# Performance work log

Hardware: AMD Instinct MI355X
Metric: run time of the kernel (lower is better)

Reference implementation:

```python
import jax, jax.numpy as jnp
import numpy as np

B, S, E, H = 2, 2048, 1024, 16
D = E // H  # head_dim = 64


def setup_inputs() -> dict:
    key = jax.random.key(0)
    ks = jax.random.split(key, 6)
    sc = 1.0 / np.sqrt(D)
    return {
        "x": jax.random.normal(ks[0], (B, S, E), dtype=jnp.float32),
        "Wq": jax.random.normal(ks[1], (D, D), dtype=jnp.float32) * sc,
        "Wk": jax.random.normal(ks[2], (D, D), dtype=jnp.float32) * sc,
        "Wv": jax.random.normal(ks[3], (D, D), dtype=jnp.float32) * sc,
        "Wo": jax.random.normal(ks[4], (E, E), dtype=jnp.float32) * (1.0 / np.sqrt(E)),
        "bo": jnp.zeros((E,), dtype=jnp.float32),
    }


def reference(x, Wq, Wk, Wv, Wo, bo):
    b, s, e = x.shape
    # split into heads: (B, H, S, D)
    xh = x.reshape(b, s, H, D).transpose(0, 2, 1, 3)
    # per-head linear projections (weights SHARED across heads); torch Linear: x @ W^T
    q = jnp.einsum('bhsd,ed->bhse', xh, Wq)
    k = jnp.einsum('bhsd,ed->bhse', xh, Wk)
    v = jnp.einsum('bhsd,ed->bhse', xh, Wv)
    # full attention matrix (B, H, S, S) — faithful to the naive original
    energy = jnp.einsum('bhqd,bhkd->bhqk', q, k)
    attn = jax.nn.softmax(energy / jnp.sqrt(jnp.asarray(D, x.dtype)), axis=-1)
    out = jnp.einsum('bhqk,bhkd->bhqd', attn, v)
    out = out.transpose(0, 2, 1, 3).reshape(b, s, e)
    return out @ Wo.T + bo
```

## Files before the change

kernel.cpp:

```cpp
#include <hip/hip_runtime.h>
#include <hip/hip_bf16.h>

#define B 2
#define S 2048
#define E 1024
#define H 16
#define D 64

typedef unsigned short ushort_t;
typedef __attribute__((ext_vector_type(8))) short bf16x8;
typedef __attribute__((ext_vector_type(4))) float f32x4;
typedef __attribute__((ext_vector_type(16))) float f32x16;

static __device__ __forceinline__ ushort_t f2bf(float f) {
    union { float f; unsigned u; } v; v.f = f;
    unsigned r = v.u + 0x7fffu + ((v.u >> 16) & 1u);
    return (ushort_t)(r >> 16);
}

#define MFMA(a, b, c)   __builtin_amdgcn_mfma_f32_16x16x32_bf16((a), (b), (c), 0, 0, 0)
#define MFMA32(a, b, c) __builtin_amdgcn_mfma_f32_32x32x16_bf16((a), (b), (c), 0, 0, 0)
#define PACKBF(hi, lo) __builtin_amdgcn_perm((hi), (lo), 0x07060302u)

__global__ __launch_bounds__(256) void cvt_w(
    const float* __restrict__ Wq, const float* __restrict__ Wk, const float* __restrict__ Wv,
    const float* __restrict__ Wo,
    ushort_t* __restrict__ wqb, ushort_t* __restrict__ wkb, ushort_t* __restrict__ wvb,
    ushort_t* __restrict__ wob)
{
    int gid = blockIdx.x, t = threadIdx.x;
    if (gid < 1024) {
        int i = gid * 1024 + t * 4;
        float4 f = *(const float4*)(Wo + i);
        ushort4 u; u.x = f2bf(f.x); u.y = f2bf(f.y); u.z = f2bf(f.z); u.w = f2bf(f.w);
        *(ushort4*)(wob + i) = u;
    } else {
        int idx = (gid - 1024) * 1024 + t * 4;
        int which = idx >> 12, off = idx & 4095;
        const float* src = (which == 0) ? Wq : (which == 1) ? Wk : Wv;
        ushort_t* dst    = (which == 0) ? wqb : (which == 1) ? wkb : wvb;
        float sc = (which == 0) ? 0.18033688011112042f : 1.0f;
        float4 f = *(const float4*)(src + off);
        ushort4 u; u.x = f2bf(f.x * sc); u.y = f2bf(f.y * sc);
        u.z = f2bf(f.z * sc); u.w = f2bf(f.w * sc);
        *(ushort4*)(dst + off) = u;
    }
}

__global__ __launch_bounds__(256) void qkv_proj(
    const float* __restrict__ x,
    const ushort_t* __restrict__ wq, const ushort_t* __restrict__ wk, const ushort_t* __restrict__ wv,
    ushort_t* __restrict__ q, ushort_t* __restrict__ k, ushort_t* __restrict__ vT)
{
    __shared__ ushort_t Xs[64][72];
    __shared__ ushort_t Wqs[64][72], Wks[64][72], Wvs[64][72];
    int t = threadIdx.x;
    int bh = blockIdx.y, b = bh >> 4, h = bh & 15;
    int s0 = blockIdx.x * 64;

    {
        int i = t >> 2, d0 = (t & 3) * 16;
        const float* xp = x + ((size_t)(b * S + s0 + i)) * E + h * D + d0;
        #pragma unroll
        for (int c = 0; c < 16; c += 4) {
            float4 f = *(const float4*)(xp + c);
            Xs[i][d0 + c + 0] = f2bf(f.x); Xs[i][d0 + c + 1] = f2bf(f.y);
            Xs[i][d0 + c + 2] = f2bf(f.z); Xs[i][d0 + c + 3] = f2bf(f.w);
        }
    }
    {
        int e = t >> 2, d0 = (t & 3) * 16;
        *(bf16x8*)&Wqs[e][d0]     = *(const bf16x8*)(wq + e * 64 + d0);
        *(bf16x8*)&Wqs[e][d0 + 8] = *(const bf16x8*)(wq + e * 64 + d0 + 8);
        *(bf16x8*)&Wks[e][d0]     = *(const bf16x8*)(wk + e * 64 + d0);
        *(bf16x8*)&Wks[e][d0 + 8] = *(const bf16x8*)(wk + e * 64 + d0 + 8);
        *(bf16x8*)&Wvs[e][d0]     = *(const bf16x8*)(wv + e * 64 + d0);
        *(bf16x8*)&Wvs[e][d0 + 8] = *(const bf16x8*)(wv + e * 64 + d0 + 8);
    }
    __syncthreads();

    int w = t >> 6, lane = t & 63, m = lane & 15, quad = lane >> 4;
    bf16x8 a0 = *(bf16x8*)&Xs[16 * w + m][quad * 8];
    bf16x8 a1 = *(bf16x8*)&Xs[16 * w + m][32 + quad * 8];
    f32x4 cq[4], ck[4], cv[4];
    #pragma unroll
    for (int nt = 0; nt < 4; nt++) { cq[nt] = (f32x4)0.f; ck[nt] = (f32x4)0.f; cv[nt] = (f32x4)0.f; }
    #pragma unroll
    for (int nt = 0; nt < 4; nt++) {
        bf16x8 b0, b1;
        b0 = *(bf16x8*)&Wqs[nt * 16 + m][quad * 8]; b1 = *(bf16x8*)&Wqs[nt * 16 + m][32 + quad * 8];
        cq[nt] = MFMA(a0, b0, cq[nt]); cq[nt] = MFMA(a1, b1, cq[nt]);
        b0 = *(bf16x8*)&Wks[nt * 16 + m][quad * 8]; b1 = *(bf16x8*)&Wks[nt * 16 + m][32 + quad * 8];
        ck[nt] = MFMA(a0, b0, ck[nt]); ck[nt] = MFMA(a1, b1, ck[nt]);
        b0 = *(bf16x8*)&Wvs[nt * 16 + m][quad * 8]; b1 = *(bf16x8*)&Wvs[nt * 16 + m][32 + quad * 8];
        cv[nt] = MFMA(a0, b0, cv[nt]); cv[nt] = MFMA(a1, b1, cv[nt]);
    }
    size_t base = (size_t)bh * S + s0;
    #pragma unroll
    for (int nt = 0; nt < 4; nt++)
        #pragma unroll
        for (int r = 0; r < 4; r++) {
            size_t idx = (base + 16 * w + quad * 4 + r) * D + nt * 16 + m;
            q[idx] = f2bf(cq[nt][r]);
            k[idx] = f2bf(ck[nt][r]);
        }
    __syncthreads();
    #pragma unroll
    for (int nt = 0; nt < 4; nt++)
        #pragma unroll
        for (int r = 0; r < 4; r++)
            Wvs[nt * 16 + m][16 * w + quad * 4 + r] = f2bf(cv[nt][r]);
    __syncthreads();
    {
        int d0 = t >> 2, sc = (t & 3) * 16;
        ushort_t* vp = vT + ((size_t)bh * D + d0) * S + s0 + sc;
        *(bf16x8*)(vp)     = *(bf16x8*)&Wvs[d0][sc];
        *(bf16x8*)(vp + 8) = *(bf16x8*)&Wvs[d0][sc + 8];
    }
}

__global__ __launch_bounds__(256) void flash_attn(
    const ushort_t* __restrict__ q, const ushort_t* __restrict__ k,
    const ushort_t* __restrict__ vT, ushort_t* __restrict__ ao)
{
    __shared__ ushort_t Ks[2][64][72];
    __shared__ ushort_t Vt[2][64][72];
    int t = threadIdx.x;
    int bh = blockIdx.y, b = bh >> 4, h = bh & 15;
    int q0 = blockIdx.x * 128;
    int w = t >> 6, lane = t & 63, l31 = lane & 31, half = lane >> 5;

    const ushort_t* qb = q + ((size_t)bh * S + q0) * D;
    const ushort_t* kb = k + (size_t)bh * S * D;
    const ushort_t* vb = vT + (size_t)bh * D * S;

    bf16x8 qf[4];
    {
        const ushort_t* qp = qb + (size_t)(w * 32 + l31) * D + half * 8;
        #pragma unroll
        for (int c = 0; c < 4; c++) qf[c] = *(const bf16x8*)(qp + c * 16);
    }

    f32x16 o0 = (f32x16)0.f, o1 = (f32x16)0.f;
    float2 ls2 = make_float2(0.f, 0.f);

    int sr = t >> 2, scc = (t & 3) * 16;
    bf16x8 kp0, kp1, vp0, vp1;

    {
        const ushort_t* kp = kb + (size_t)sr * D + scc;
        const ushort_t* vp = vb + (size_t)sr * S + scc;
        kp0 = *(const bf16x8*)(kp);     kp1 = *(const bf16x8*)(kp + 8);
        vp0 = *(const bf16x8*)(vp);     vp1 = *(const bf16x8*)(vp + 8);
        *(bf16x8*)&Ks[0][sr][scc]     = kp0;
        *(bf16x8*)&Ks[0][sr][scc + 8] = kp1;
        *(bf16x8*)&Vt[0][sr][scc]     = vp0;
        *(bf16x8*)&Vt[0][sr][scc + 8] = vp1;
    }
    __syncthreads();
    {
        const ushort_t* kp = kb + (size_t)(64 + sr) * D + scc;
        const ushort_t* vp = vb + (size_t)sr * S + 64 + scc;
        kp0 = *(const bf16x8*)(kp);     kp1 = *(const bf16x8*)(kp + 8);
        vp0 = *(const bf16x8*)(vp);     vp1 = *(const bf16x8*)(vp + 8);
    }

    const int NT = S / 64;
    for (int it = 0; it < NT; it++) {
        int p = it & 1;
        if (it + 1 < NT) {
            *(bf16x8*)&Ks[1 - p][sr][scc]     = kp0;
            *(bf16x8*)&Ks[1 - p][sr][scc + 8] = kp1;
            *(bf16x8*)&Vt[1 - p][sr][scc]     = vp0;
            *(bf16x8*)&Vt[1 - p][sr][scc + 8] = vp1;
        }
        if (it + 2 < NT) {
            int k0n = (it + 2) * 64;
            const ushort_t* kp = kb + (size_t)(k0n + sr) * D + scc;
            const ushort_t* vp = vb + (size_t)sr * S + k0n + scc;
            kp0 = *(const bf16x8*)(kp);     kp1 = *(const bf16x8*)(kp + 8);
            vp0 = *(const bf16x8*)(vp);     vp1 = *(const bf16x8*)(vp + 8);
        }

        union { unsigned u[4]; bf16x8 v; } pa[4];
        #pragma unroll
        for (int st = 0; st < 2; st++) {
            f32x16 e = (f32x16)0.f;
            #pragma unroll
            for (int c = 0; c < 4; c++) {
                bf16x8 ka = *(bf16x8*)&Ks[p][st * 32 + l31][c * 16 + half * 8];
                e = MFMA32(ka, qf[c], e);
            }
            unsigned pt[16];
            #pragma unroll
            for (int r = 0; r < 16; r += 2) {
                float pe0 = __builtin_amdgcn_exp2f(e[r]);
                float pe1 = __builtin_amdgcn_exp2f(e[r + 1]);
                ls2.x += pe0; ls2.y += pe1;
                pt[r]     = __float_as_uint(pe0);
                pt[r + 1] = __float_as_uint(pe1);
            }
            #pragma unroll
            for (int c2 = 0; c2 < 2; c2++) {
                int rb = c2 * 8;
                unsigned dA = PACKBF(pt[rb + 1], pt[rb + 0]);
                unsigned dB = PACKBF(pt[rb + 3], pt[rb + 2]);
                unsigned dC = PACKBF(pt[rb + 5], pt[rb + 4]);
                unsigned dD = PACKBF(pt[rb + 7], pt[rb + 6]);
                unsigned x1 = (unsigned)__shfl_xor((int)(half ? dA : dC), 32, 64);
                unsigned x2 = (unsigned)__shfl_xor((int)(half ? dB : dD), 32, 64);
                int kc = st * 2 + c2;
                pa[kc].u[0] = half ? x1 : dA;
                pa[kc].u[1] = half ? x2 : dB;
                pa[kc].u[2] = half ? dC : x1;
                pa[kc].u[3] = half ? dD : x2;
            }
        }

        #pragma unroll
        for (int kc = 0; kc < 4; kc++) {
            bf16x8 vf0 = *(bf16x8*)&Vt[p][l31][kc * 16 + half * 8];
            bf16x8 vf1 = *(bf16x8*)&Vt[p][32 + l31][kc * 16 + half * 8];
            o0 = MFMA32(pa[kc].v, vf0, o0);
            o1 = MFMA32(pa[kc].v, vf1, o1);
        }
        __syncthreads();
    }

    float lsum = ls2.x + ls2.y;
    float lfull = lsum + __shfl_xor(lsum, 32, 64);
    float inv = 1.001953125f / lfull;
    #pragma unroll
    for (int reg = 0; reg < 16; reg++) {
        int qrow = (reg & 3) + 8 * (reg >> 2) + 4 * half;
        float li = __shfl(inv, qrow, 64);
        int srow = q0 + w * 32 + qrow;
        size_t base = ((size_t)(b * S + srow)) * E + h * D + l31;
        ao[base]      = f2bf(o0[reg] * li);
        ao[base + 32] = f2bf(o1[reg] * li);
    }
}

__global__ __launch_bounds__(256) void out_proj(
    const ushort_t* __restrict__ A, const ushort_t* __restrict__ Wob,
    const float* __restrict__ bo, float* __restrict__ Y)
{
    __shared__ ushort_t As[2][128][72];
    __shared__ ushort_t Ws[2][64][72];
    int t = threadIdx.x;
    int n0 = blockIdx.x * 64, m0 = blockIdx.y * 128;
    int w = t >> 6, lane = t & 63, m = lane & 15, quad = lane >> 4;
    f32x4 acc[2][4];
    #pragma unroll
    for (int u = 0; u < 2; u++)
        #pragma unroll
        for (int nt = 0; nt < 4; nt++) acc[u][nt] = (f32x4)0.f;

    int ar = t >> 1, ac = (t & 1) * 32;
    int wr = t >> 2, wc = (t & 3) * 16;
    const ushort_t* apb = A + (size_t)(m0 + ar) * E + ac;
    const ushort_t* wpb = Wob + (size_t)(n0 + wr) * E + wc;

    bf16x8 arg[4], wrg[2];
    {
        #pragma unroll
        for (int i = 0; i < 4; i++) *(bf16x8*)&As[0][ar][ac + 8 * i] = *(const bf16x8*)(apb + 8 * i);
        *(bf16x8*)&Ws[0][wr][wc]     = *(const bf16x8*)(wpb);
        *(bf16x8*)&Ws[0][wr][wc + 8] = *(const bf16x8*)(wpb + 8);
    }
    __syncthreads();
    {
        #pragma unroll
        for (int i = 0; i < 4; i++) arg[i] = *(const bf16x8*)(apb + 64 + 8 * i);
        wrg[0] = *(const bf16x8*)(wpb + 64);
        wrg[1] = *(const bf16x8*)(wpb + 64 + 8);
    }

    const int KT = E / 64;
    for (int ks = 0; ks < KT; ks++) {
        int p = ks & 1;
        if (ks + 1 < KT) {
            #pragma unroll
            for (int i = 0; i < 4; i++) *(bf16x8*)&As[1 - p][ar][ac + 8 * i] = arg[i];
            *(bf16x8*)&Ws[1 - p][wr][wc]     = wrg[0];
            *(bf16x8*)&Ws[1 - p][wr][wc + 8] = wrg[1];
        }
        if (ks + 2 < KT) {
            int off = (ks + 2) * 64;
            #pragma unroll
            for (int i = 0; i < 4; i++) arg[i] = *(const bf16x8*)(apb + off + 8 * i);
            wrg[0] = *(const bf16x8*)(wpb + off);
            wrg[1] = *(const bf16x8*)(wpb + off + 8);
        }
        #pragma unroll
        for (int h2 = 0; h2 < 2; h2++) {
            bf16x8 af[2];
            af[0] = *(bf16x8*)&As[p][w * 32 + m][h2 * 32 + quad * 8];
            af[1] = *(bf16x8*)&As[p][w * 32 + 16 + m][h2 * 32 + quad * 8];
            #pragma unroll
            for (int nt = 0; nt < 4; nt++) {
                bf16x8 bfr = *(bf16x8*)&Ws[p][nt * 16 + m][h2 * 32 + quad * 8];
                acc[0][nt] = MFMA(af[0], bfr, acc[0][nt]);
                acc[1][nt] = MFMA(af[1], bfr, acc[1][nt]);
            }
        }
        __syncthreads();
    }
    #pragma unroll
    for (int u = 0; u < 2; u++)
        #pragma unroll
        for (int nt = 0; nt < 4; nt++)
            #pragma unroll
            for (int r = 0; r < 4; r++) {
                int row = m0 + w * 32 + u * 16 + quad * 4 + r;
                int col = n0 + nt * 16 + m;
                Y[(size_t)row * E + col] = acc[u][nt][r] + bo[col];
            }
}

extern "C" void kernel_launch(void* const* d_in, const int* in_sizes, int n_in,
                              void* d_out, int out_size, void* d_ws, size_t ws_size,
                              hipStream_t stream)
{
    const float* x  = (const float*)d_in[0];
    const float* Wq = (const float*)d_in[1];
    const float* Wk = (const float*)d_in[2];
    const float* Wv = (const float*)d_in[3];
    const float* Wo = (const float*)d_in[4];
    const float* bo = (const float*)d_in[5];
    float* Y = (float*)d_out;

    const size_t n = (size_t)B * H * S * D;
    ushort_t* qw  = (ushort_t*)d_ws;
    ushort_t* kw  = qw + n;
    ushort_t* vTw = kw + n;
    ushort_t* ao  = vTw + n;
    ushort_t* wob = ao + n;
    ushort_t* wqb = wob + (size_t)E * E;
    ushort_t* wkb = wqb + D * D;
    ushort_t* wvb = wkb + D * D;

    cvt_w<<<dim3(1024 + 12), 256, 0, stream>>>(Wq, Wk, Wv, Wo, wqb, wkb, wvb, wob);
    qkv_proj<<<dim3(S / 64, B * H), 256, 0, stream>>>(x, wqb, wkb, wvb, qw, kw, vTw);
    flash_attn<<<dim3(S / 128, B * H), 256, 0, stream>>>(qw, kw, vTw, ao);
    out_proj<<<dim3(E / 64, (B * S) / 128), 256, 0, stream>>>(ao, wob, bo, Y);
}
```

Measured before the change: 150.6 us.

## Split key range across two wave groups in flash attention and merge via LDS

```diff
diff --git a/kernel.cpp b/kernel.cpp
--- a/kernel.cpp
+++ b/kernel.cpp
@@ -119,16 +119,18 @@
     }
 }
 
-__global__ __launch_bounds__(256) void flash_attn(
+__global__ __launch_bounds__(512, 4) void flash_attn(
     const ushort_t* __restrict__ q, const ushort_t* __restrict__ k,
     const ushort_t* __restrict__ vT, ushort_t* __restrict__ ao)
 {
-    __shared__ ushort_t Ks[2][64][72];
-    __shared__ ushort_t Vt[2][64][72];
+    __shared__ ushort_t Ks[2][2][64][72];
+    __shared__ ushort_t Vt[2][2][64][72];
     int t = threadIdx.x;
     int bh = blockIdx.y, b = bh >> 4, h = bh & 15;
     int q0 = blockIdx.x * 128;
     int w = t >> 6, lane = t & 63, l31 = lane & 31, half = lane >> 5;
+    int g = w >> 2, wq = w & 3;
+    int tg = t & 255;
 
     const ushort_t* qb = q + ((size_t)bh * S + q0) * D;
     const ushort_t* kb = k + (size_t)bh * S * D;
@@ -136,7 +138,7 @@
 
     bf16x8 qf[4];
     {
-        const ushort_t* qp = qb + (size_t)(w * 32 + l31) * D + half * 8;
+        const ushort_t* qp = qb + (size_t)(wq * 32 + l31) * D + half * 8;
         #pragma unroll
         for (int c = 0; c < 4; c++) qf[c] = *(const bf16x8*)(qp + c * 16);
     }
@@ -144,38 +146,40 @@
     f32x16 o0 = (f32x16)0.f, o1 = (f32x16)0.f;
     float2 ls2 = make_float2(0.f, 0.f);
 
-    int sr = t >> 2, scc = (t & 3) * 16;
+    int sr = tg >> 2, scc = (tg & 3) * 16;
     bf16x8 kp0, kp1, vp0, vp1;
 
     {
-        const ushort_t* kp = kb + (size_t)sr * D + scc;
-        const ushort_t* vp = vb + (size_t)sr * S + scc;
+        int k00 = g * 64;
+        const ushort_t* kp = kb + (size_t)(k00 + sr) * D + scc;
+        const ushort_t* vp = vb + (size_t)sr * S + k00 + scc;
         kp0 = *(const bf16x8*)(kp);     kp1 = *(const bf16x8*)(kp + 8);
         vp0 = *(const bf16x8*)(vp);     vp1 = *(const bf16x8*)(vp + 8);
-        *(bf16x8*)&Ks[0][sr][scc]     = kp0;
-        *(bf16x8*)&Ks[0][sr][scc + 8] = kp1;
-        *(bf16x8*)&Vt[0][sr][scc]     = vp0;
-        *(bf16x8*)&Vt[0][sr][scc + 8] = vp1;
-    }
-    __syncthreads();
-    {
-        const ushort_t* kp = kb + (size_t)(64 + sr) * D + scc;
-        const ushort_t* vp = vb + (size_t)sr * S + 64 + scc;
+        *(bf16x8*)&Ks[g][0][sr][scc]     = kp0;
+        *(bf16x8*)&Ks[g][0][sr][scc + 8] = kp1;
+        *(bf16x8*)&Vt[g][0][sr][scc]     = vp0;
+        *(bf16x8*)&Vt[g][0][sr][scc + 8] = vp1;
+    }
+    __syncthreads();
+    {
+        int k01 = (2 + g) * 64;
+        const ushort_t* kp = kb + (size_t)(k01 + sr) * D + scc;
+        const ushort_t* vp = vb + (size_t)sr * S + k01 + scc;
         kp0 = *(const bf16x8*)(kp);     kp1 = *(const bf16x8*)(kp + 8);
         vp0 = *(const bf16x8*)(vp);     vp1 = *(const bf16x8*)(vp + 8);
     }
 
-    const int NT = S / 64;
-    for (int it = 0; it < NT; it++) {
-        int p = it & 1;
-        if (it + 1 < NT) {
-            *(bf16x8*)&Ks[1 - p][sr][scc]     = kp0;
-            *(bf16x8*)&Ks[1 - p][sr][scc + 8] = kp1;
-            *(bf16x8*)&Vt[1 - p][sr][scc]     = vp0;
-            *(bf16x8*)&Vt[1 - p][sr][scc + 8] = vp1;
-        }
-        if (it + 2 < NT) {
-            int k0n = (it + 2) * 64;
+    const int NJ = S / 128;
+    for (int jt = 0; jt < NJ; jt++) {
+        int p = jt & 1;
+        if (jt + 1 < NJ) {
+            *(bf16x8*)&Ks[g][1 - p][sr][scc]     = kp0;
+            *(bf16x8*)&Ks[g][1 - p][sr][scc + 8] = kp1;
+            *(bf16x8*)&Vt[g][1 - p][sr][scc]     = vp0;
+            *(bf16x8*)&Vt[g][1 - p][sr][scc + 8] = vp1;
+        }
+        if (jt + 2 < NJ) {
+            int k0n = (2 * (jt + 2) + g) * 64;
             const ushort_t* kp = kb + (size_t)(k0n + sr) * D + scc;
             const ushort_t* vp = vb + (size_t)sr * S + k0n + scc;
             kp0 = *(const bf16x8*)(kp);     kp1 = *(const bf16x8*)(kp + 8);
@@ -188,7 +192,7 @@
             f32x16 e = (f32x16)0.f;
             #pragma unroll
             for (int c = 0; c < 4; c++) {
-                bf16x8 ka = *(bf16x8*)&Ks[p][st * 32 + l31][c * 16 + half * 8];
+                bf16x8 ka = *(bf16x8*)&Ks[g][p][st * 32 + l31][c * 16 + half * 8];
                 e = MFMA32(ka, qf[c], e);
             }
             unsigned pt[16];
@@ -219,8 +223,8 @@
 
         #pragma unroll
         for (int kc = 0; kc < 4; kc++) {
-            bf16x8 vf0 = *(bf16x8*)&Vt[p][l31][kc * 16 + half * 8];
-            bf16x8 vf1 = *(bf16x8*)&Vt[p][32 + l31][kc * 16 + half * 8];
+            bf16x8 vf0 = *(bf16x8*)&Vt[g][p][l31][kc * 16 + half * 8];
+            bf16x8 vf1 = *(bf16x8*)&Vt[g][p][32 + l31][kc * 16 + half * 8];
             o0 = MFMA32(pa[kc].v, vf0, o0);
             o1 = MFMA32(pa[kc].v, vf1, o1);
         }
@@ -228,16 +232,29 @@
     }
 
     float lsum = ls2.x + ls2.y;
-    float lfull = lsum + __shfl_xor(lsum, 32, 64);
-    float inv = 1.001953125f / lfull;
-    #pragma unroll
-    for (int reg = 0; reg < 16; reg++) {
-        int qrow = (reg & 3) + 8 * (reg >> 2) + 4 * half;
-        float li = __shfl(inv, qrow, 64);
-        int srow = q0 + w * 32 + qrow;
-        size_t base = ((size_t)(b * S + srow)) * E + h * D + l31;
-        ao[base]      = f2bf(o0[reg] * li);
-        ao[base + 32] = f2bf(o1[reg] * li);
+    float* cmb = (float*)&Ks[0][0][0][0];
+    int slot = (wq * 64 + lane) * 33;
+    if (g == 1) {
+        #pragma unroll
+        for (int r2 = 0; r2 < 16; r2++) { cmb[slot + r2] = o0[r2]; cmb[slot + 16 + r2] = o1[r2]; }
+        cmb[slot + 32] = lsum;
+    }
+    __syncthreads();
+    if (g == 0) {
+        #pragma unroll
+        for (int r2 = 0; r2 < 16; r2++) { o0[r2] += cmb[slot + r2]; o1[r2] += cmb[slot + 16 + r2]; }
+        lsum += cmb[slot + 32];
+        float lfull = lsum + __shfl_xor(lsum, 32, 64);
+        float inv = 1.001953125f / lfull;
+        #pragma unroll
+        for (int reg = 0; reg < 16; reg++) {
+            int qrow = (reg & 3) + 8 * (reg >> 2) + 4 * half;
+            float li = __shfl(inv, qrow, 64);
+            int srow = q0 + wq * 32 + qrow;
+            size_t base2 = ((size_t)(b * S + srow)) * E + h * D + l31;
+            ao[base2]      = f2bf(o0[reg] * li);
+            ao[base2 + 32] = f2bf(o1[reg] * li);
+        }
     }
 }
 
@@ -342,6 +359,6 @@
 
     cvt_w<<<dim3(1024 + 12), 256, 0, stream>>>(Wq, Wk, Wv, Wo, wqb, wkb, wvb, wob);
     qkv_proj<<<dim3(S / 64, B * H), 256, 0, stream>>>(x, wqb, wkb, wvb, qw, kw, vTw);
-    flash_attn<<<dim3(S / 128, B * H), 256, 0, stream>>>(qw, kw, vTw, ao);
+    flash_attn<<<dim3(S / 128, B * H), 512, 0, stream>>>(qw, kw, vTw, ao);
     out_proj<<<dim3(E / 64, (B * S) / 128), 256, 0, stream>>>(ao, wob, bo, Y);
 }
```

After: 146.7 us. -2.6%, faster.
